# Kernel optimization log

Hardware: AMD Instinct MI355X
Metric: run time of the kernel (lower is better)

## Reference

```python
import jax, jax.numpy as jnp
import numpy as np

L = 1.0          # diffusion coefficient `l`
CHUNK = 1024     # tile size over the blurred-pixel axis


def _conv(x, k):
    # x: [B,H,W,C], k: [kh,kw,C,F] -> [B,H,W,F]; equivalent to the source's
    # NCHW/OIHW transposed conv with 'SAME' padding, stride 1.
    return jax.lax.conv_general_dilated(
        x, k, window_strides=(1, 1), padding='SAME',
        dimension_numbers=('NHWC', 'HWIO', 'NHWC'))


def _difference(x, blurred):
    # difference[b,i,j,k] = sum_{p,q,f} tanh(x[b,i,j,k] - blurred[b,p,q,f])
    # Computed in CHUNK-sized tiles over the blurred axis to avoid the
    # [B, H*W*C, H*W*F] all-pairs tensor the nested vmaps would materialize.
    b = x.shape[0]
    xf = x.reshape(b, -1)                              # [B, M]
    yf = blurred.reshape(b, -1)                        # [B, N]
    n = yf.shape[1]
    pad = (-n) % CHUNK
    yf = jnp.pad(yf, ((0, 0), (0, pad)))
    mask = jnp.pad(jnp.ones((n,), x.dtype), (0, pad))
    ychunks = yf.reshape(b, -1, CHUNK).transpose(1, 0, 2)   # [S, B, CHUNK]
    mchunks = mask.reshape(-1, CHUNK)                        # [S, CHUNK]

    def step(acc, ym):
        yc, mc = ym
        d = jnp.tanh(xf[:, :, None] - yc[:, None, :])        # [B, M, CHUNK]
        return acc + jnp.einsum('bmn,n->bm', d, mc), None

    acc, _ = jax.lax.scan(step, jnp.zeros_like(xf), (ychunks, mchunks))
    return acc.reshape(x.shape)                              # [B,H,W,C]


def setup_inputs() -> dict:
    key = jax.random.key(0)
    k1, k2, k3, k4 = jax.random.split(key, 4)
    lecun = 1.0 / np.sqrt(5 * 5 * 3)  # fan_in of the 5x5x3 kernels
    return {
        'inputs': jax.random.normal(k1, (2, 32, 32, 3), dtype=jnp.float32),
        'm': jax.random.normal(k2, (5, 5, 3, 16), dtype=jnp.float32) * lecun,
        'w': jax.random.normal(k3, (5, 5, 3, 16), dtype=jnp.float32) * lecun,
        'g': jax.random.normal(k4, (5, 5, 3, 16), dtype=jnp.float32) * lecun,
    }


def reference(inputs, m, w, g):
    first_term = _conv(inputs, m)          # [B,H,W,F]
    blurred = _conv(inputs, g)             # [B,H,W,F]
    difference = _difference(inputs, blurred)  # [B,H,W,C]
    second_term = _conv(difference, w)     # [B,H,W,F]
    return first_term - L * second_term
```

## Files before the change

kernel.cpp:

```cpp
#include <hip/hip_runtime.h>

#define BB 2
#define HH 32
#define WW 32
#define CC 3
#define FF 16
#define M_PER_B (HH*WW*CC)
#define N_PER_B (HH*WW*FF)
#define CHN 256
#define NQUADS (CHN/4)
#define NCHUNKS (N_PER_B / CHN)
#define MPT 2
#define MBLOCKS (M_PER_B / (256*MPT))

__global__ __launch_bounds__(256) void diff_kernel(
    const float* __restrict__ x,
    const float* __restrict__ gk,
    float* __restrict__ dacc)
{
    __shared__ float Fs[CHN];
    __shared__ __align__(16) float Es[NQUADS*8];
    const int tid = threadIdx.x;
    const int b   = blockIdx.z;
    const int mb  = blockIdx.x;
    const int nc  = blockIdx.y;

    const int m0 = mb * (256*MPT) + tid;
    const int m1 = m0 + 256;
    const float E0 = __expf(2.0f * x[b*M_PER_B + m0]);
    const float E1 = __expf(2.0f * x[b*M_PER_B + m1]);

    {
        int n = nc * CHN + tid;
        int p = n >> 9;
        int r = n & 511;
        int q = r >> 4;
        int f = r & 15;
        float acc = 0.f;
        #pragma unroll
        for (int dh = 0; dh < 5; ++dh) {
            int hh = p + dh - 2;
            if ((unsigned)hh >= (unsigned)HH) continue;
            #pragma unroll
            for (int dw = 0; dw < 5; ++dw) {
                int ww = q + dw - 2;
                if ((unsigned)ww >= (unsigned)WW) continue;
                const float* xin = x  + ((b*HH + hh)*WW + ww)*CC;
                const float* gg  = gk + ((dh*5 + dw)*CC)*FF + f;
                #pragma unroll
                for (int c = 0; c < CC; ++c)
                    acc += xin[c] * gg[c*FF];
            }
        }
        Fs[tid] = __expf(-2.0f * acc);
    }
    __syncthreads();

    if (tid < NQUADS) {
        float f0 = Fs[4*tid+0], f1 = Fs[4*tid+1];
        float f2 = Fs[4*tid+2], f3 = Fs[4*tid+3];
        float s01 = f0 + f1, s23 = f2 + f3;
        float p01 = f0 * f1, p23 = f2 * f3;
        float e1 = s01 + s23;
        float e2 = p01 + p23 + s01 * s23;
        float e3 = p01 * s23 + p23 * s01;
        float e4 = p01 * p23;
        float* e = &Es[8*tid];
        e[0] = e1; e[1] = e2; e[2] = e3; e[3] = e4;
        e[4] = 3.0f * e1; e[5] = 2.0f * e2;
    }
    __syncthreads();

    float s0 = 0.f, s1 = 0.f;
    #pragma unroll 4
    for (int q = 0; q < NQUADS; ++q) {
        const float4 d  = *(const float4*)(&Es[8*q]);
        const float2 nv = *(const float2*)(&Es[8*q+4]);
        float num0 = fmaf(fmaf(fmaf(d.z, E0, nv.y), E0, nv.x), E0, 4.0f);
        float den0 = fmaf(fmaf(fmaf(fmaf(d.w, E0, d.z), E0, d.y), E0, d.x), E0, 1.0f);
        s0 = fmaf(num0, __builtin_amdgcn_rcpf(den0), s0);
        float num1 = fmaf(fmaf(fmaf(d.z, E1, nv.y), E1, nv.x), E1, 4.0f);
        float den1 = fmaf(fmaf(fmaf(fmaf(d.w, E1, d.z), E1, d.y), E1, d.x), E1, 1.0f);
        s1 = fmaf(num1, __builtin_amdgcn_rcpf(den1), s1);
    }
    atomicAdd(&dacc[b*M_PER_B + m0], -2.0f * s0);
    atomicAdd(&dacc[b*M_PER_B + m1], -2.0f * s1);
}

__global__ __launch_bounds__(256) void out_kernel(
    const float* __restrict__ x,
    const float* __restrict__ mker,
    const float* __restrict__ wker,
    const float* __restrict__ dacc,
    float* __restrict__ out)
{
    int o = blockIdx.x * 256 + threadIdx.x;
    int f = o & 15;
    int t = o >> 4;
    int j = t & 31;  t >>= 5;
    int i = t & 31;  t >>= 5;
    int b = t;
    float ft = 0.f, st = 0.f;
    #pragma unroll
    for (int dh = 0; dh < 5; ++dh) {
        int hh = i + dh - 2;
        if ((unsigned)hh >= (unsigned)HH) continue;
        #pragma unroll
        for (int dw = 0; dw < 5; ++dw) {
            int ww = j + dw - 2;
            if ((unsigned)ww >= (unsigned)WW) continue;
            int base = ((b*HH + hh)*WW + ww)*CC;
            int kb   = ((dh*5 + dw)*CC)*FF + f;
            #pragma unroll
            for (int c = 0; c < CC; ++c) {
                ft += x[base + c] * mker[kb + c*FF];
                st += (16384.0f + dacc[base + c]) * wker[kb + c*FF];
            }
        }
    }
    out[o] = ft - st;
}

extern "C" void kernel_launch(void* const* d_in, const int* in_sizes, int n_in,
                              void* d_out, int out_size, void* d_ws, size_t ws_size,
                              hipStream_t stream) {
    const float* x  = (const float*)d_in[0];
    const float* mk = (const float*)d_in[1];
    const float* wk = (const float*)d_in[2];
    const float* gk = (const float*)d_in[3];
    float* out  = (float*)d_out;
    float* dacc = (float*)d_ws;

    diff_kernel<<<dim3(MBLOCKS, NCHUNKS, BB), 256, 0, stream>>>(x, gk, dacc);
    out_kernel<<<(BB*HH*WW*FF)/256, 256, 0, stream>>>(x, mk, wk, dacc, out);
}
```

Measured before the change: 79.47 us.

## Replace atomic accumulation with per-chunk partials reduced in the output kernel

The diff kernel now writes its per-chunk tanh sums to a separate partial buffer slice instead of calling atomicAdd on a shared accumulator. The output kernel changes to one block per half-row. Each block sums the 64 partials for its 5x20x3 input halo into LDS, then runs the conv from LDS. This removes contended atomics and the dependence on a pre-zeroed workspace. In exchange it needs a much larger workspace, adds strided partial reads, and launches far fewer output blocks.

```diff
diff --git a/kernel.cpp b/kernel.cpp
--- a/kernel.cpp
+++ b/kernel.cpp
@@ -16,7 +16,7 @@
 __global__ __launch_bounds__(256) void diff_kernel(
     const float* __restrict__ x,
     const float* __restrict__ gk,
-    float* __restrict__ dacc)
+    float* __restrict__ part)
 {
     __shared__ float Fs[CHN];
     __shared__ __align__(16) float Es[NQUADS*8];
@@ -83,23 +83,55 @@
         float den1 = fmaf(fmaf(fmaf(fmaf(d.w, E1, d.z), E1, d.y), E1, d.x), E1, 1.0f);
         s1 = fmaf(num1, __builtin_amdgcn_rcpf(den1), s1);
     }
-    atomicAdd(&dacc[b*M_PER_B + m0], -2.0f * s0);
-    atomicAdd(&dacc[b*M_PER_B + m1], -2.0f * s1);
+    float* p = part + ((size_t)nc * BB + b) * M_PER_B;
+    p[m0] = -2.0f * s0;
+    p[m1] = -2.0f * s1;
 }
 
 __global__ __launch_bounds__(256) void out_kernel(
     const float* __restrict__ x,
     const float* __restrict__ mker,
     const float* __restrict__ wker,
-    const float* __restrict__ dacc,
+    const float* __restrict__ part,
     float* __restrict__ out)
 {
-    int o = blockIdx.x * 256 + threadIdx.x;
-    int f = o & 15;
-    int t = o >> 4;
-    int j = t & 31;  t >>= 5;
-    int i = t & 31;  t >>= 5;
-    int b = t;
+    __shared__ float dlds[5*20*3];
+    const int blk = blockIdx.x;
+    const int tid = threadIdx.x;
+    const int jh = blk & 1;
+    const int i  = (blk >> 1) & 31;
+    const int b  = blk >> 6;
+    const int j0 = jh * 16;
+
+    for (int v = tid; v < 5*20*3; v += 256) {
+        int c  = v % 3;
+        int t  = v / 3;
+        int dj = t % 20;
+        int dh = t / 20;
+        int hh = i + dh - 2;
+        int ww = j0 + dj - 2;
+        float val = 0.f;
+        if ((unsigned)hh < (unsigned)HH && (unsigned)ww < (unsigned)WW) {
+            int m = (hh*WW + ww)*CC + c;
+            const float* p = part + (size_t)b * M_PER_B + m;
+            const int stride = BB * M_PER_B;
+            float a0 = 0.f, a1 = 0.f, a2 = 0.f, a3 = 0.f;
+            #pragma unroll 4
+            for (int nc = 0; nc < NCHUNKS; nc += 4) {
+                a0 += p[(size_t)(nc+0) * stride];
+                a1 += p[(size_t)(nc+1) * stride];
+                a2 += p[(size_t)(nc+2) * stride];
+                a3 += p[(size_t)(nc+3) * stride];
+            }
+            val = 16384.0f + ((a0 + a1) + (a2 + a3));
+        }
+        dlds[v] = val;
+    }
+    __syncthreads();
+
+    const int f  = tid & 15;
+    const int jj = tid >> 4;
+    const int j  = j0 + jj;
     float ft = 0.f, st = 0.f;
     #pragma unroll
     for (int dh = 0; dh < 5; ++dh) {
@@ -110,15 +142,16 @@
             int ww = j + dw - 2;
             if ((unsigned)ww >= (unsigned)WW) continue;
             int base = ((b*HH + hh)*WW + ww)*CC;
+            int lb   = (dh*20 + (jj + dw))*3;
             int kb   = ((dh*5 + dw)*CC)*FF + f;
             #pragma unroll
             for (int c = 0; c < CC; ++c) {
                 ft += x[base + c] * mker[kb + c*FF];
-                st += (16384.0f + dacc[base + c]) * wker[kb + c*FF];
+                st += dlds[lb + c] * wker[kb + c*FF];
             }
         }
     }
-    out[o] = ft - st;
+    out[(((b*HH + i)*WW + j)*FF) + f] = ft - st;
 }
 
 extern "C" void kernel_launch(void* const* d_in, const int* in_sizes, int n_in,
@@ -129,8 +162,8 @@
     const float* wk = (const float*)d_in[2];
     const float* gk = (const float*)d_in[3];
     float* out  = (float*)d_out;
-    float* dacc = (float*)d_ws;
+    float* part = (float*)d_ws;
 
-    diff_kernel<<<dim3(MBLOCKS, NCHUNKS, BB), 256, 0, stream>>>(x, gk, dacc);
-    out_kernel<<<(BB*HH*WW*FF)/256, 256, 0, stream>>>(x, mk, wk, dacc, out);
+    diff_kernel<<<dim3(MBLOCKS, NCHUNKS, BB), 256, 0, stream>>>(x, gk, part);
+    out_kernel<<<(BB*HH*2), 256, 0, stream>>>(x, mk, wk, part, out);
 }
```

Result: slower. 86.08 us (+8.3%).
